# Optimization experiments

Measured on AMD Instinct MI355X. Metric: run time of the kernel, lower is better.

The kernel has to match this reference:

```python
import jax, jax.numpy as jnp
import numpy as np

N_PULSES = 8_000_000
NUM_DOMS = 200_000
EPS = 1e-08


def setup_inputs() -> dict:
    key = jax.random.key(0)
    k1, k2, k3 = jax.random.split(key, 3)
    times = jax.random.normal(k1, (N_PULSES,), dtype=jnp.float32) * 100.0
    charges = jax.random.uniform(k2, (N_PULSES,), dtype=jnp.float32) * 10.0
    dom_idx = jax.random.randint(k3, (N_PULSES,), 0, NUM_DOMS, dtype=jnp.int32)
    return {"times": times, "charges": charges, "dom_idx": dom_idx, "num_doms": NUM_DOMS}


def reference(times, charges, dom_idx, num_doms):
    n = times.shape[0]
    ones = jnp.ones_like(times)
    # per-DOM pulse counts (float, matching torch's float scatter_add of ones)
    count = jnp.zeros((num_doms,), dtype=times.dtype).at[dom_idx].add(ones)

    # --- temporal features ---
    first_times = jnp.full((num_doms,), jnp.inf, dtype=times.dtype).at[dom_idx].min(times)
    delta_t_first = times - first_times[dom_idx]

    mean_times = jnp.zeros((num_doms,), dtype=times.dtype).at[dom_idx].add(times) / (count + EPS)
    mean_e = mean_times[dom_idx]
    delta_t_median = times - mean_e

    var = jnp.zeros((num_doms,), dtype=times.dtype).at[dom_idx].add((times - mean_e) ** 2) / (count + EPS)
    time_std = jnp.sqrt(var + EPS)
    t_normalized = (times - mean_e) / (time_std[dom_idx] + EPS)

    # --- charge features ---
    total_charges = jnp.zeros((num_doms,), dtype=charges.dtype).at[dom_idx].add(charges)
    charge_fraction = charges / (total_charges[dom_idx] + EPS)

    max_charges = jnp.full((num_doms,), -jnp.inf, dtype=charges.dtype).at[dom_idx].max(charges)
    charge_ratio = charges / (max_charges[dom_idx] + EPS)

    # --- charge rank within each DOM (0 = brightest), fully vectorized ---
    # sort primarily by dom_idx, secondarily by descending charge
    order = jnp.lexsort((-charges, dom_idx))  # (n,)
    sorted_dom = dom_idx[order]
    counts_i = jnp.zeros((num_doms,), dtype=jnp.int32).at[dom_idx].add(jnp.ones_like(dom_idx))
    starts = jnp.cumsum(counts_i) - counts_i  # exclusive prefix-sum of group sizes
    rank_sorted = jnp.arange(n, dtype=jnp.int32) - starts[sorted_dom]
    ranks = jnp.zeros((n,), dtype=jnp.int32).at[order].set(rank_sorted)

    dom_sizes_e = count[dom_idx]  # float sizes per pulse
    log_charge_rank = jnp.log((ranks.astype(times.dtype) + 1.0) / (dom_sizes_e + EPS))

    return jnp.stack(
        [delta_t_first, delta_t_median, t_normalized,
         charge_fraction, charge_ratio, log_charge_rank], axis=1)
```

## Files before the change

### kernel.cpp

```cpp
#include <hip/hip_runtime.h>
#include <hip/hip_bf16.h>
#include <stdint.h>
#include <math.h>

#define NDOMS 200000
#define EPSF 1e-8f
#define DLBITS 8
#define DLMASK 255
#define NBUCK ((NDOMS + DLMASK) >> DLBITS)
#define CAP_B 11264
#define CAP_H 6144
#define CHUNK 8192
#define IDXM 0x7FFFFFu

typedef unsigned long long u64;

__device__ __forceinline__ unsigned f2mono(float f){
  unsigned b = __float_as_uint(f);
  return b ^ (unsigned)(((int)b >> 31) | 0x80000000);
}
__device__ __forceinline__ float mono2f(unsigned u){
  unsigned b = (u & 0x80000000u) ? (u ^ 0x80000000u) : ~u;
  return __uint_as_float(b);
}

__global__ void k_init(int* __restrict__ gcursor){
  int i = blockIdx.x * blockDim.x + threadIdx.x;
  if (i < NBUCK) gcursor[i] = 0;
}

__global__ void __launch_bounds__(512)
k_bin(const float* __restrict__ charges, const int* __restrict__ dom,
      const float* __restrict__ times, int n, int* __restrict__ gcursor,
      uint4* __restrict__ rec_g){
  __shared__ int lhist[NBUCK];
  __shared__ int lbase[NBUCK];
  __shared__ int lcnt[NBUCK];
  int t = threadIdx.x;
  int start = blockIdx.x * CHUNK;
  int end = min(start + CHUNK, n);
  for (int i = t; i < NBUCK; i += 512) lhist[i] = 0;
  __syncthreads();
  for (int p = start + t; p < end; p += 512)
    atomicAdd(&lhist[dom[p] >> DLBITS], 1);
  __syncthreads();
  for (int i = t; i < NBUCK; i += 512){
    int c = lhist[i];
    lbase[i] = c ? atomicAdd(&gcursor[i], c) : 0;
    lcnt[i] = 0;
  }
  __syncthreads();
  for (int p = start + t; p < end; p += 512){
    int d = dom[p];
    int b = d >> DLBITS;
    int pos = lbase[b] + atomicAdd(&lcnt[b], 1);
    if (pos < CAP_B){
      uint4 r;
      r.x = ((unsigned)(d & DLMASK) << 23) | (IDXM - (unsigned)p);
      r.y = __float_as_uint(charges[p]);
      r.z = __float_as_uint(times[p]);
      r.w = (unsigned)d;
      rec_g[(size_t)b * CAP_B + pos] = r;
    }
  }
}

__global__ void __launch_bounds__(512)
k_grp(const uint4* __restrict__ rec_g, const int* __restrict__ gcursor,
      float* __restrict__ derived, unsigned char* __restrict__ rank8p){
  __shared__ u64   keysL[CAP_H];
  __shared__ int hist[128], starts[128], cur[128];
  __shared__ float s_t[128], s_t2[128], s_c[128];
  __shared__ unsigned mn_t[128], mx_c[128];
  __shared__ int s_tot;
  int b = blockIdx.x >> 1, h = blockIdx.x & 1, t = threadIdx.x;
  int cnt = gcursor[b];
  if (cnt > CAP_B) cnt = CAP_B;
  const uint4* rg = rec_g + (size_t)b * CAP_B;

  if (t < 128){
    hist[t] = 0; s_t[t] = 0.f; s_t2[t] = 0.f; s_c[t] = 0.f;
    mn_t[t] = 0xFFFFFFFFu; mx_c[t] = 0u;
  }
  __syncthreads();
  for (int s = t; s < cnt; s += 512){
    int dg = (int)((rg[s].x >> 23) & DLMASK);
    if ((dg >> 7) == h) atomicAdd(&hist[dg & 127], 1);
  }
  __syncthreads();
  if (t < 128) starts[t] = hist[t];
  __syncthreads();
  for (int off = 1; off < 128; off <<= 1){
    int v = 0;
    if (t < 128 && t >= off) v = starts[t - off];
    __syncthreads();
    if (t < 128) starts[t] += v;
    __syncthreads();
  }
  if (t < 128){ starts[t] -= hist[t]; cur[t] = starts[t]; }
  if (t == 127) s_tot = starts[127] + hist[127];
  __syncthreads();
  for (int s = t; s < cnt; s += 512){
    uint4 r = rg[s];
    int dg = (int)((r.x >> 23) & DLMASK);
    if ((dg >> 7) != h) continue;
    int dl = dg & 127;
    float tv = __uint_as_float(r.z);
    int pos = atomicAdd(&cur[dl], 1);
    if (pos < CAP_H) keysL[pos] = ((u64)r.y << 32) | r.x;
    atomicAdd(&s_t[dl], tv);
    atomicAdd(&s_t2[dl], tv * tv);
    atomicAdd(&s_c[dl], __uint_as_float(r.y));
    atomicMax(&mx_c[dl], r.y);
    atomicMin(&mn_t[dl], f2mono(tv));
  }
  __syncthreads();
  if (t < 128){
    int k = hist[t];
    if (k > 0){
      int d = b * 256 + h * 128 + t;
      float kf = (float)k;
      float m  = s_t[t] / (kf + EPSF);
      float var = (s_t2[t] - 2.0f * m * s_t[t] + kf * m * m) / (kf + EPSF);
      var = fmaxf(var, 0.0f);
      float* dv = derived + (size_t)d * 8;
      dv[0] = mono2f(mn_t[t]);
      dv[1] = m;
      dv[2] = 1.0f / (sqrtf(var + EPSF) + EPSF);
      dv[3] = 1.0f / (s_c[t] + EPSF);
      dv[4] = 1.0f / (__uint_as_float(mx_c[t]) + EPSF);
      dv[5] = kf; dv[6] = 0.f; dv[7] = 0.f;
    }
  }
  int tot = min(s_tot, CAP_H);
  for (int s = t; s < tot; s += 512){
    u64 me = keysL[s];
    int dl = (int)((me >> 23) & 127);
    int st = starts[dl], k = hist[dl];
    int r = 0;
    for (int j = st; j < st + k; ++j) r += (keysL[j] > me) ? 1 : 0;
    rank8p[IDXM - (unsigned)(me & IDXM)] = (unsigned char)r;
  }
}

__global__ void __launch_bounds__(256)
k_out(const float* __restrict__ times, const float* __restrict__ charges,
      const int* __restrict__ dom, const unsigned char* __restrict__ rank8p,
      const float* __restrict__ derived, int n, float* __restrict__ out){
  __shared__ float st[1536];
  int b = blockIdx.x, t = threadIdx.x;
  int p = b * 256 + t;
  float f[6] = {0.f, 0.f, 0.f, 0.f, 0.f, 0.f};
  if (p < n){
    float tv = times[p], cv = charges[p];
    int d = dom[p];
    float r = (float)rank8p[p];
    const float4* dv = (const float4*)(derived + (size_t)d * 8);
    float4 d0 = dv[0];
    float4 d1 = dv[1];
    float dm = tv - d0.y;
    f[0] = tv - d0.x;
    f[1] = dm;
    f[2] = dm * d0.z;
    f[3] = cv * d0.w;
    f[4] = cv * d1.x;
    f[5] = logf((r + 1.0f) / (d1.y + EPSF));
  }
  if ((b + 1) * 256 <= n){
    #pragma unroll
    for (int j = 0; j < 6; ++j) st[t * 6 + j] = f[j];
    __syncthreads();
    float* ob = out + (size_t)b * 1536;
    #pragma unroll
    for (int j = 0; j < 6; ++j) ob[j * 256 + t] = st[j * 256 + t];
  } else if (p < n){
    for (int j = 0; j < 6; ++j) out[(size_t)p * 6 + j] = f[j];
  }
}

extern "C" void kernel_launch(void* const* d_in, const int* in_sizes, int n_in,
                              void* d_out, int out_size, void* d_ws, size_t ws_size,
                              hipStream_t stream) {
  const float* times   = (const float*)d_in[0];
  const float* charges = (const float*)d_in[1];
  const int*   dom     = (const int*)d_in[2];
  const int n = in_sizes[0];

  char* w = (char*)d_ws;
  int*   gcursor = (int*)w;   w += ((size_t)NBUCK * 4 + 255) & ~255ull;
  float* derived = (float*)w; w += (size_t)NDOMS * 32;
  unsigned char* rank8p = (unsigned char*)w; w += (size_t)n;

  uint4* rec_g = (uint4*)d_out;

  k_init<<<(NBUCK + 255) / 256, 256, 0, stream>>>(gcursor);
  k_bin<<<(n + CHUNK - 1) / CHUNK, 512, 0, stream>>>(charges, dom, times, n,
                                                     gcursor, rec_g);
  k_grp<<<NBUCK * 2, 512, 0, stream>>>(rec_g, gcursor, derived, rank8p);
  k_out<<<(n + 255) / 256, 256, 0, stream>>>(times, charges, dom, rank8p,
                                             derived, n, (float*)d_out);
}
```

Before: 796.4 us.

## Bin records per half-bucket from both ends so group blocks read only their own records

The binning pass now keeps separate cursors for each 128-DOM half-bucket, padded to separate cache lines. The low half is written from the front of the shared bucket region and the high half from the back. Each grouping block therefore reads only its own records, once, and holds them in registers to build both the statistics and the sort keys. Before, both half-blocks scanned the whole bucket twice. The change adds more global atomic cursors and a fixed register-held cap of 12 records per thread, with CAP_H lowered to fit.

```diff
diff --git a/kernel.cpp b/kernel.cpp
--- a/kernel.cpp
+++ b/kernel.cpp
@@ -8,8 +8,10 @@
 #define DLBITS 8
 #define DLMASK 255
 #define NBUCK ((NDOMS + DLMASK) >> DLBITS)
+#define NB2 (NBUCK * 2)
 #define CAP_B 11264
-#define CAP_H 6144
+#define CAP_H 6016
+#define CSTRIDE 16
 #define CHUNK 8192
 #define IDXM 0x7FFFFFu
 
@@ -26,41 +28,43 @@
 
 __global__ void k_init(int* __restrict__ gcursor){
   int i = blockIdx.x * blockDim.x + threadIdx.x;
-  if (i < NBUCK) gcursor[i] = 0;
+  if (i < NB2) gcursor[i * CSTRIDE] = 0;
 }
 
 __global__ void __launch_bounds__(512)
 k_bin(const float* __restrict__ charges, const int* __restrict__ dom,
       const float* __restrict__ times, int n, int* __restrict__ gcursor,
       uint4* __restrict__ rec_g){
-  __shared__ int lhist[NBUCK];
-  __shared__ int lbase[NBUCK];
-  __shared__ int lcnt[NBUCK];
+  __shared__ int lhist[NB2];
+  __shared__ int lbase[NB2];
+  __shared__ int lcnt[NB2];
   int t = threadIdx.x;
   int start = blockIdx.x * CHUNK;
   int end = min(start + CHUNK, n);
-  for (int i = t; i < NBUCK; i += 512) lhist[i] = 0;
+  for (int i = t; i < NB2; i += 512) lhist[i] = 0;
   __syncthreads();
   for (int p = start + t; p < end; p += 512)
-    atomicAdd(&lhist[dom[p] >> DLBITS], 1);
-  __syncthreads();
-  for (int i = t; i < NBUCK; i += 512){
+    atomicAdd(&lhist[dom[p] >> 7], 1);
+  __syncthreads();
+  for (int i = t; i < NB2; i += 512){
     int c = lhist[i];
-    lbase[i] = c ? atomicAdd(&gcursor[i], c) : 0;
+    lbase[i] = c ? atomicAdd(&gcursor[i * CSTRIDE], c) : 0;
     lcnt[i] = 0;
   }
   __syncthreads();
   for (int p = start + t; p < end; p += 512){
     int d = dom[p];
-    int b = d >> DLBITS;
-    int pos = lbase[b] + atomicAdd(&lcnt[b], 1);
+    int i2 = d >> 7;
+    int pos = lbase[i2] + atomicAdd(&lcnt[i2], 1);
     if (pos < CAP_B){
+      int b = i2 >> 1;
+      int slot = (i2 & 1) ? (CAP_B - 1 - pos) : pos;
       uint4 r;
       r.x = ((unsigned)(d & DLMASK) << 23) | (IDXM - (unsigned)p);
       r.y = __float_as_uint(charges[p]);
       r.z = __float_as_uint(times[p]);
       r.w = (unsigned)d;
-      rec_g[(size_t)b * CAP_B + pos] = r;
+      rec_g[(size_t)b * CAP_B + slot] = r;
     }
   }
 }
@@ -72,20 +76,35 @@
   __shared__ int hist[128], starts[128], cur[128];
   __shared__ float s_t[128], s_t2[128], s_c[128];
   __shared__ unsigned mn_t[128], mx_c[128];
-  __shared__ int s_tot;
-  int b = blockIdx.x >> 1, h = blockIdx.x & 1, t = threadIdx.x;
-  int cnt = gcursor[b];
-  if (cnt > CAP_B) cnt = CAP_B;
-  const uint4* rg = rec_g + (size_t)b * CAP_B;
+  int bid = blockIdx.x, b = bid >> 1, h = bid & 1, t = threadIdx.x;
+  int cl = min(gcursor[(2 * b) * CSTRIDE], CAP_B);
+  int ch = min(gcursor[(2 * b + 1) * CSTRIDE], CAP_B - cl);
+  int myCnt  = h ? ch : cl;
+  if (myCnt > CAP_H) myCnt = CAP_H;
+  int myBase = h ? (CAP_B - ch) : 0;
+  const uint4* rg = rec_g + (size_t)b * CAP_B + myBase;
 
   if (t < 128){
     hist[t] = 0; s_t[t] = 0.f; s_t2[t] = 0.f; s_c[t] = 0.f;
     mn_t[t] = 0xFFFFFFFFu; mx_c[t] = 0u;
   }
   __syncthreads();
-  for (int s = t; s < cnt; s += 512){
-    int dg = (int)((rg[s].x >> 23) & DLMASK);
-    if ((dg >> 7) == h) atomicAdd(&hist[dg & 127], 1);
+  unsigned rx[12], ry[12], rz[12];
+  #pragma unroll
+  for (int i = 0; i < 12; ++i){
+    int s = t + i * 512;
+    if (s < myCnt){
+      uint4 r = rg[s];
+      rx[i] = r.x; ry[i] = r.y; rz[i] = r.z;
+      int dl = (int)((r.x >> 23) & 127);
+      float tv = __uint_as_float(r.z);
+      atomicAdd(&hist[dl], 1);
+      atomicAdd(&s_t[dl], tv);
+      atomicAdd(&s_t2[dl], tv * tv);
+      atomicAdd(&s_c[dl], __uint_as_float(r.y));
+      atomicMax(&mx_c[dl], r.y);
+      atomicMin(&mn_t[dl], f2mono(tv));
+    }
   }
   __syncthreads();
   if (t < 128) starts[t] = hist[t];
@@ -98,21 +117,15 @@
     __syncthreads();
   }
   if (t < 128){ starts[t] -= hist[t]; cur[t] = starts[t]; }
-  if (t == 127) s_tot = starts[127] + hist[127];
-  __syncthreads();
-  for (int s = t; s < cnt; s += 512){
-    uint4 r = rg[s];
-    int dg = (int)((r.x >> 23) & DLMASK);
-    if ((dg >> 7) != h) continue;
-    int dl = dg & 127;
-    float tv = __uint_as_float(r.z);
-    int pos = atomicAdd(&cur[dl], 1);
-    if (pos < CAP_H) keysL[pos] = ((u64)r.y << 32) | r.x;
-    atomicAdd(&s_t[dl], tv);
-    atomicAdd(&s_t2[dl], tv * tv);
-    atomicAdd(&s_c[dl], __uint_as_float(r.y));
-    atomicMax(&mx_c[dl], r.y);
-    atomicMin(&mn_t[dl], f2mono(tv));
+  __syncthreads();
+  #pragma unroll
+  for (int i = 0; i < 12; ++i){
+    int s = t + i * 512;
+    if (s < myCnt){
+      int dl = (int)((rx[i] >> 23) & 127);
+      int pos = atomicAdd(&cur[dl], 1);
+      keysL[pos] = ((u64)ry[i] << 32) | rx[i];
+    }
   }
   __syncthreads();
   if (t < 128){
@@ -132,8 +145,7 @@
       dv[5] = kf; dv[6] = 0.f; dv[7] = 0.f;
     }
   }
-  int tot = min(s_tot, CAP_H);
-  for (int s = t; s < tot; s += 512){
+  for (int s = t; s < myCnt; s += 512){
     u64 me = keysL[s];
     int dl = (int)((me >> 23) & 127);
     int st = starts[dl], k = hist[dl];
@@ -187,16 +199,16 @@
   const int n = in_sizes[0];
 
   char* w = (char*)d_ws;
-  int*   gcursor = (int*)w;   w += ((size_t)NBUCK * 4 + 255) & ~255ull;
+  int*   gcursor = (int*)w;   w += ((size_t)NB2 * CSTRIDE * 4 + 255) & ~255ull;
   float* derived = (float*)w; w += (size_t)NDOMS * 32;
   unsigned char* rank8p = (unsigned char*)w; w += (size_t)n;
 
   uint4* rec_g = (uint4*)d_out;
 
-  k_init<<<(NBUCK + 255) / 256, 256, 0, stream>>>(gcursor);
+  k_init<<<(NB2 + 255) / 256, 256, 0, stream>>>(gcursor);
   k_bin<<<(n + CHUNK - 1) / CHUNK, 512, 0, stream>>>(charges, dom, times, n,
                                                      gcursor, rec_g);
-  k_grp<<<NBUCK * 2, 512, 0, stream>>>(rec_g, gcursor, derived, rank8p);
+  k_grp<<<NB2, 512, 0, stream>>>(rec_g, gcursor, derived, rank8p);
   k_out<<<(n + 255) / 256, 256, 0, stream>>>(times, charges, dom, rank8p,
                                              derived, n, (float*)d_out);
 }
```

Measured after the change: 817.3 us. 2.6% more time.
